# Optimization experiments

Hardware: AMD Instinct MI355X
Metric: run time of the kernel (lower is better)

## Reference

```python
import jax, jax.numpy as jnp
import numpy as np

B, T, D = 64, 512, 512
H, DH = 8, 64  # head_num, att_embedding_size; H*DH == D
NEG = jnp.float32(-2.0**32 + 1)


def _pos_encoding(t, d):
    # Position_Embedding (mode='sum'): [cos, sin] concat over d/2 frequencies
    inv_freq = 1.0 / jnp.power(10000.0, 2.0 * jnp.arange(d // 2, dtype=jnp.float32) / d)
    pij = jnp.arange(t, dtype=jnp.float32)[:, None] * inv_freq[None, :]  # (T, d/2)
    return jnp.concatenate([jnp.cos(pij), jnp.sin(pij)], axis=-1)  # (T, d)


def setup_inputs() -> dict:
    key = jax.random.key(0)
    ks = jax.random.split(key, 9)
    queries = jax.random.normal(ks[0], (B, T, D), dtype=jnp.float32)
    keys = jax.random.normal(ks[1], (B, T, D), dtype=jnp.float32)
    query_lens = jax.random.randint(ks[2], (B, 1), 1, T + 1)
    key_lens = jax.random.randint(ks[3], (B, 1), 1, T + 1)
    W_Q = jax.random.truncated_normal(ks[4], -2., 2., (D, H * DH), dtype=jnp.float32) * 0.05
    W_K = jax.random.truncated_normal(ks[5], -2., 2., (D, H * DH), dtype=jnp.float32) * 0.05
    W_V = jax.random.truncated_normal(ks[6], -2., 2., (D, H * DH), dtype=jnp.float32) * 0.05
    fw1 = jax.random.normal(ks[7], (H * DH, 4 * H * DH), dtype=jnp.float32) * 0.02
    fw2 = jax.random.normal(ks[8], (4 * H * DH, H * DH), dtype=jnp.float32) * 0.02
    return {"queries": queries, "keys": keys, "query_lens": query_lens,
            "key_lens": key_lens, "W_Q": W_Q, "W_K": W_K, "W_V": W_V,
            "fw1": fw1, "fw2": fw2}


def reference(queries, keys, query_lens, key_lens, W_Q, W_K, W_V, fw1, fw2):
    # sequence masks (B, T) from lengths (B, 1)
    ar = jnp.arange(T)
    q_mask = (ar[None, :] < query_lens).astype(jnp.float32)  # (B, T)
    k_mask = ar[None, :] < key_lens                          # (B, T) bool

    pe = _pos_encoding(T, D)[None]  # (1, T, D)
    q_in = queries + pe
    k_in = keys + pe

    qp = jnp.einsum('btd,de->bte', q_in, W_Q).reshape(B, T, H, DH)
    kp = jnp.einsum('btd,de->bte', k_in, W_K)
    # DeepCTR quirk: values projected from the already-projected keys
    vp = jnp.einsum('btd,de->bte', kp, W_V).reshape(B, T, H, DH)
    kp = kp.reshape(B, T, H, DH)

    scores = jnp.einsum('bthd,bshd->bhts', qp, kp) / jnp.sqrt(jnp.float32(DH))
    scores = jnp.where(k_mask[:, None, None, :], scores, NEG)
    scores = scores - jnp.max(scores, axis=-1, keepdims=True)
    attn = jax.nn.softmax(scores, axis=-1)
    attn = attn * q_mask[:, None, :, None]

    out = jnp.einsum('bhts,bshd->bthd', attn, vp).reshape(B, T, H * DH)
    result = out + q_in  # residual uses PE-augmented queries

    ff = jnp.einsum('btd,df->btf', jax.nn.relu(jnp.einsum('btd,df->btf', result, fw1)), fw2)
    result = result + ff

    return jnp.mean(result, axis=1, keepdims=True)  # (B, 1, D)
```

## Files before the change

kernel.cpp:

```cpp
#include <hip/hip_runtime.h>

typedef unsigned short u16;
typedef __attribute__((ext_vector_type(8))) short short8;
typedef __attribute__((ext_vector_type(4))) float floatx4;

#define QSCALE 0.1803368801111204f

__device__ __forceinline__ u16 f2bf(float x) {
  union { float f; unsigned u; } un; un.f = x;
  unsigned r = un.u + 0x7fffu + ((un.u >> 16) & 1u);
  return (u16)(r >> 16);
}
__device__ __forceinline__ float bf2f(u16 h) {
  union { unsigned u; float f; } un; un.u = ((unsigned)h) << 16;
  return un.f;
}
__device__ __forceinline__ void gld16(const u16* g, u16* l) {
  __builtin_amdgcn_global_load_lds((__attribute__((address_space(1))) void*)g,
                                   (__attribute__((address_space(3))) void*)l, 16, 0, 0);
}

__global__ __launch_bounds__(256) void wtrans_all(const float* __restrict__ W_Q,
                                                  const float* __restrict__ W_K,
                                                  const float* __restrict__ fw1,
                                                  u16* __restrict__ WqT, u16* __restrict__ WkT,
                                                  u16* __restrict__ F1T) {
  __shared__ float tile[32][33];
  int L = blockIdx.x;
  const float* in;
  u16* out;
  int N, bx, by;
  if (L < 256) { in = W_Q; out = WqT; N = 512; bx = L & 15; by = L >> 4; }
  else if (L < 512) { L -= 256; in = W_K; out = WkT; N = 512; bx = L & 15; by = L >> 4; }
  else { L -= 512; in = fw1; out = F1T; N = 2048; bx = L & 63; by = L >> 6; }
  int tx = threadIdx.x, ty = threadIdx.y;
  int n0 = bx * 32, k0 = by * 32;
#pragma unroll
  for (int i = 0; i < 4; i++) {
    int kk = ty + i * 8;
    tile[kk][tx] = in[(size_t)(k0 + kk) * N + n0 + tx];
  }
  __syncthreads();
#pragma unroll
  for (int i = 0; i < 4; i++) {
    int nn = ty + i * 8;
    out[(size_t)(n0 + nn) * 512 + k0 + tx] = f2bf(tile[tx][nn]);
  }
}

__global__ __launch_bounds__(256) void wkv_kernel(const float* __restrict__ WK,
                                                  const float* __restrict__ WV,
                                                  u16* __restrict__ WkvT) {
  __shared__ float Kt[32][36];
  __shared__ float Vt[32][36];
  int nt = blockIdx.x & 15, dt = blockIdx.x >> 4;
  int n0 = nt * 32, d0 = dt * 32;
  int tid = threadIdx.x;
  int flat = tid * 4;
  int i4 = flat >> 5, j4 = flat & 31;
  int tn = tid & 15, td = tid >> 4;
  float acc00 = 0.f, acc01 = 0.f, acc10 = 0.f, acc11 = 0.f;
  for (int e0 = 0; e0 < 512; e0 += 32) {
    __syncthreads();
    *(float4*)&Kt[i4][j4] = *(const float4*)&WK[(size_t)(d0 + i4) * 512 + e0 + j4];
    *(float4*)&Vt[i4][j4] = *(const float4*)&WV[(size_t)(e0 + i4) * 512 + n0 + j4];
    __syncthreads();
#pragma unroll 8
    for (int e = 0; e < 32; e++) {
      float k0v = Kt[td * 2][e], k1v = Kt[td * 2 + 1][e];
      float v0 = Vt[e][tn * 2], v1 = Vt[e][tn * 2 + 1];
      acc00 += k0v * v0; acc01 += k0v * v1;
      acc10 += k1v * v0; acc11 += k1v * v1;
    }
  }
  size_t o = (size_t)(n0 + tn * 2) * 512 + d0 + td * 2;
  WkvT[o] = f2bf(acc00);
  WkvT[o + 1] = f2bf(acc10);
  WkvT[o + 512] = f2bf(acc01);
  WkvT[o + 513] = f2bf(acc11);
}

__global__ __launch_bounds__(256) void pe_table_kernel(float* __restrict__ pet) {
  int flat = (blockIdx.x * 256 + threadIdx.x) * 4;
  int d0 = flat & 511;
  int t = flat >> 9;
  float pe[4];
#pragma unroll
  for (int i = 0; i < 4; i++) {
    int d = d0 + i;
    int j = (d < 256) ? d : d - 256;
    float f = exp2f((float)j * -0.05190512648f);
    float arg = (float)t * f;
    pe[i] = (d < 256) ? cosf(arg) : sinf(arg);
  }
  *(float4*)(pet + flat) = *(const float4*)pe;
}

__global__ __launch_bounds__(256) void pe_add_kernel(const float* __restrict__ q,
                                                     const float* __restrict__ k,
                                                     const float* __restrict__ pet,
                                                     u16* __restrict__ qb, u16* __restrict__ kb) {
  size_t flat = ((size_t)blockIdx.x * 256 + threadIdx.x) * 4;
  const float4 qv = *(const float4*)(q + flat);
  const float4 kv = *(const float4*)(k + flat);
  const float4 pv = *(const float4*)(pet + (flat & 262143));
  u16 qo[4], ko[4];
  qo[0] = f2bf(qv.x + pv.x); qo[1] = f2bf(qv.y + pv.y);
  qo[2] = f2bf(qv.z + pv.z); qo[3] = f2bf(qv.w + pv.w);
  ko[0] = f2bf(kv.x + pv.x); ko[1] = f2bf(kv.y + pv.y);
  ko[2] = f2bf(kv.z + pv.z); ko[3] = f2bf(kv.w + pv.w);
  *(uint2*)(qb + flat) = *(const uint2*)qo;
  *(uint2*)(kb + flat) = *(const uint2*)ko;
}

__global__ __launch_bounds__(512, 2) void proj_256(const u16* __restrict__ q_in,
                                                   const u16* __restrict__ k_in,
                                                   const u16* __restrict__ WqT,
                                                   const u16* __restrict__ WkT,
                                                   const u16* __restrict__ WkvT,
                                                   u16* __restrict__ qp,
                                                   u16* __restrict__ kpb,
                                                   u16* __restrict__ vTp) {
  __shared__ u16 lds[65536];
  const int K = 512;
  const int tid = threadIdx.x;
  const int lane = tid & 63, w = tid >> 6;
  const int quad = lane >> 4, cl = lane & 15;
  const int wm = w >> 2, wn = w & 3;
  int L = blockIdx.x;
  const int seg = L >> 8;
  L &= 255;
  const u16* A = (seg == 0) ? q_in : k_in;
  const u16* Bt = (seg == 0) ? WqT : (seg == 1) ? WkT : WkvT;
  const int xcd = L & 7, s = L >> 3;
  const int nx = s & 1;
  const int rgrp = s >> 1;
  const int tm = (rgrp * 8 + xcd) * 256;
  const int tn = nx * 256;
  const int srow = lane >> 3;
  const int sg = (lane & 7) ^ srow;
  const int cb = w * 4;

  floatx4 acc[8][4] = {};

  {
    u16* Ab = lds;
    u16* Bb = lds + 16384;
#pragma unroll
    for (int i = 0; i < 4; i++) {
      int cc = cb + i, row = cc * 8 + srow;
      gld16(A + ((size_t)(tm + row) * K + sg * 8), &Ab[cc * 512]);
    }
#pragma unroll
    for (int i = 0; i < 4; i++) {
      int cc = cb + i, row = cc * 8 + srow;
      gld16(Bt + ((size_t)(tn + row) * K + sg * 8), &Bb[cc * 512]);
    }
  }

  const int nk = K >> 6;
#pragma unroll 1
  for (int kt = 0; kt < nk; kt++) {
    u16* Ab = lds + (kt & 1) * 32768;
    u16* Bb = Ab + 16384;
    u16* An = lds + ((kt & 1) ^ 1) * 32768;
    u16* Bn = An + 16384;
    const bool pf = (kt + 1 < nk);
    const int k0n = (kt + 1) << 6;
    if (pf) {
#pragma unroll
      for (int i = 0; i < 4; i++) {
        int cc = cb + i, row = cc * 8 + srow;
        gld16(A + ((size_t)(tm + row) * K + k0n + sg * 8), &An[cc * 512]);
      }
#pragma unroll
      for (int i = 0; i < 4; i++) {
        int cc = cb + i, row = cc * 8 + srow;
        gld16(Bt + ((size_t)(tn + row) * K + k0n + sg * 8), &Bn[cc * 512]);
      }
      asm volatile("s_waitcnt vmcnt(8)" ::: "memory");
    } else {
      asm volatile("s_waitcnt vmcnt(0)" ::: "memory");
    }
    __builtin_amdgcn_s_barrier();
    __builtin_amdgcn_sched_barrier(0);
    short8 a0[4][2], b0[2][2], b1[2][2], a1[4][2];
#pragma unroll
    for (int f = 0; f < 4; f++)
#pragma unroll
      for (int kh = 0; kh < 2; kh++)
        a0[f][kh] = *(const short8*)&Ab[(wm * 128 + f * 16 + cl) * 64 + ((((kh << 2) + quad)) ^ (cl & 7)) * 8];
#pragma unroll
    for (int n = 0; n < 2; n++)
#pragma unroll
      for (int kh = 0; kh < 2; kh++)
        b0[n][kh] = *(const short8*)&Bb[(wn * 64 + n * 16 + cl) * 64 + ((((kh << 2) + quad)) ^ (cl & 7)) * 8];
#pragma unroll
    for (int f = 0; f < 4; f++)
#pragma unroll
      for (int n = 0; n < 2; n++)
#pragma unroll
        for (int kh = 0; kh < 2; kh++)
          acc[f][n] = __builtin_amdgcn_mfma_f32_16x16x32_bf16(a0[f][kh], b0[n][kh], acc[f][n], 0, 0, 0);
#pragma unroll
    for (int n = 0; n < 2; n++)
#pragma unroll
      for (int kh = 0; kh < 2; kh++)
        b1[n][kh] = *(const short8*)&Bb[(wn * 64 + (n + 2) * 16 + cl) * 64 + ((((kh << 2) + quad)) ^ (cl & 7)) * 8];
#pragma unroll
    for (int f = 0; f < 4; f++)
#pragma unroll
      for (int n = 0; n < 2; n++)
#pragma unroll
        for (int kh = 0; kh < 2; kh++)
          acc[f][n + 2] = __builtin_amdgcn_mfma_f32_16x16x32_bf16(a0[f][kh], b1[n][kh], acc[f][n + 2], 0, 0, 0);
#pragma unroll
    for (int f = 0; f < 4; f++)
#pragma unroll
      for (int kh = 0; kh < 2; kh++)
        a1[f][kh] = *(const short8*)&Ab[(wm * 128 + (f + 4) * 16 + cl) * 64 + ((((kh << 2) + quad)) ^ (cl & 7)) * 8];
#pragma unroll
    for (int f = 0; f < 4; f++)
#pragma unroll
      for (int n = 0; n < 2; n++)
#pragma unroll
        for (int kh = 0; kh < 2; kh++)
          acc[f + 4][n + 2] = __builtin_amdgcn_mfma_f32_16x16x32_bf16(a1[f][kh], b1[n][kh], acc[f + 4][n + 2], 0, 0, 0);
#pragma unroll
    for (int f = 0; f < 4; f++)
#pragma unroll
      for (int n = 0; n < 2; n++)
#pragma unroll
        for (int kh = 0; kh < 2; kh++)
          acc[f + 4][n] = __builtin_amdgcn_mfma_f32_16x16x32_bf16(a1[f][kh], b0[n][kh], acc[f + 4][n], 0, 0, 0);
    __builtin_amdgcn_s_barrier();
  }

  if (seg < 2) {
    u16* C = (seg == 0) ? qp : kpb;
#pragma unroll
    for (int f = 0; f < 8; f++)
#pragma unroll
      for (int n = 0; n < 4; n++)
#pragma unroll
        for (int r = 0; r < 4; r++) {
          int row = tm + wm * 128 + f * 16 + quad * 4 + r;
          int col = tn + wn * 64 + n * 16 + cl;
          C[(size_t)row * 512 + col] = f2bf(acc[f][n][r]);
        }
  } else {
    const int b = tm >> 9, sbase = tm & 511;
#pragma unroll 1
    for (int p = 0; p < 2; p++) {
      __syncthreads();
      if ((wn >> 1) == p) {
        int cbase = (wn & 1) * 64;
#pragma unroll
        for (int f = 0; f < 8; f++)
#pragma unroll
          for (int n = 0; n < 4; n++)
#pragma unroll
            for (int r = 0; r < 4; r++) {
              int tc = cbase + n * 16 + cl;
              int row = wm * 128 + f * 16 + quad * 4 + r;
              lds[tc * 264 + row] = f2bf(acc[f][n][r]);
            }
      }
      __syncthreads();
      int col = tid >> 2;
      int e = tn + p * 128 + col;
      int h = e >> 6, d = e & 63;
      u16* dst = vTp + ((size_t)((b * 8 + h) * 64 + d) * 512 + sbase);
#pragma unroll
      for (int j = 0; j < 8; j++) {
        int chunk = (tid & 3) + j * 4;
        *(short8*)(dst + chunk * 8) = *(const short8*)&lds[col * 264 + chunk * 8];
      }
    }
  }
}

__global__ __launch_bounds__(512, 2) void ffn1_256(const u16* __restrict__ A,
                                                   const u16* __restrict__ Bt,
                                                   float* __restrict__ outp) {
  __shared__ u16 lds[65536];
  const int K = 512;
  const int tid = threadIdx.x;
  const int lane = tid & 63, w = tid >> 6;
  const int quad = lane >> 4, cl = lane & 15;
  const int wm = w >> 2, wn = w & 3;
  int L = blockIdx.x;
  const int xcd = L & 7, s = L >> 3;
  const int nx = s & 7;
  const int rgrp = s >> 3;
  const int tm = (rgrp * 8 + xcd) * 256;
  const int tn = nx * 256;
  const int srow = lane >> 3;
  const int sg = (lane & 7) ^ srow;
  const int cb = w * 4;

  floatx4 acc[8][4] = {};

  {
    u16* Ab = lds;
    u16* Bb = lds + 16384;
#pragma unroll
    for (int i = 0; i < 4; i++) {
      int cc = cb + i, row = cc * 8 + srow;
      gld16(A + ((size_t)(tm + row) * K + sg * 8), &Ab[cc * 512]);
    }
#pragma unroll
    for (int i = 0; i < 4; i++) {
      int cc = cb + i, row = cc * 8 + srow;
      gld16(Bt + ((size_t)(tn + row) * K + sg * 8), &Bb[cc * 512]);
    }
  }

  const int nk = K >> 6;
#pragma unroll 1
  for (int kt = 0; kt < nk; kt++) {
    u16* Ab = lds + (kt & 1) * 32768;
    u16* Bb = Ab + 16384;
    u16* An = lds + ((kt & 1) ^ 1) * 32768;
    u16* Bn = An + 16384;
    const bool pf = (kt + 1 < nk);
    const int k0n = (kt + 1) << 6;
    if (pf) {
#pragma unroll
      for (int i = 0; i < 4; i++) {
        int cc = cb + i, row = cc * 8 + srow;
        gld16(A + ((size_t)(tm + row) * K + k0n + sg * 8), &An[cc * 512]);
      }
#pragma unroll
      for (int i = 0; i < 4; i++) {
        int cc = cb + i, row = cc * 8 + srow;
        gld16(Bt + ((size_t)(tn + row) * K + k0n + sg * 8), &Bn[cc * 512]);
      }
      asm volatile("s_waitcnt vmcnt(8)" ::: "memory");
    } else {
      asm volatile("s_waitcnt vmcnt(0)" ::: "memory");
    }
    __builtin_amdgcn_s_barrier();
    __builtin_amdgcn_sched_barrier(0);
    short8 a0[4][2], b0[2][2], b1[2][2], a1[4][2];
#pragma unroll
    for (int f = 0; f < 4; f++)
#pragma unroll
      for (int kh = 0; kh < 2; kh++)
        a0[f][kh] = *(const short8*)&Ab[(wm * 128 + f * 16 + cl) * 64 + ((((kh << 2) + quad)) ^ (cl & 7)) * 8];
#pragma unroll
    for (int n = 0; n < 2; n++)
#pragma unroll
      for (int kh = 0; kh < 2; kh++)
        b0[n][kh] = *(const short8*)&Bb[(wn * 64 + n * 16 + cl) * 64 + ((((kh << 2) + quad)) ^ (cl & 7)) * 8];
#pragma unroll
    for (int f = 0; f < 4; f++)
#pragma unroll
      for (int n = 0; n < 2; n++)
#pragma unroll
        for (int kh = 0; kh < 2; kh++)
          acc[f][n] = __builtin_amdgcn_mfma_f32_16x16x32_bf16(a0[f][kh], b0[n][kh], acc[f][n], 0, 0, 0);
#pragma unroll
    for (int n = 0; n < 2; n++)
#pragma unroll
      for (int kh = 0; kh < 2; kh++)
        b1[n][kh] = *(const short8*)&Bb[(wn * 64 + (n + 2) * 16 + cl) * 64 + ((((kh << 2) + quad)) ^ (cl & 7)) * 8];
#pragma unroll
    for (int f = 0; f < 4; f++)
#pragma unroll
      for (int n = 0; n < 2; n++)
#pragma unroll
        for (int kh = 0; kh < 2; kh++)
          acc[f][n + 2] = __builtin_amdgcn_mfma_f32_16x16x32_bf16(a0[f][kh], b1[n][kh], acc[f][n + 2], 0, 0, 0);
#pragma unroll
    for (int f = 0; f < 4; f++)
#pragma unroll
      for (int kh = 0; kh < 2; kh++)
        a1[f][kh] = *(const short8*)&Ab[(wm * 128 + (f + 4) * 16 + cl) * 64 + ((((kh << 2) + quad)) ^ (cl & 7)) * 8];
#pragma unroll
    for (int f = 0; f < 4; f++)
#pragma unroll
      for (int n = 0; n < 2; n++)
#pragma unroll
        for (int kh = 0; kh < 2; kh++)
          acc[f + 4][n + 2] = __builtin_amdgcn_mfma_f32_16x16x32_bf16(a1[f][kh], b1[n][kh], acc[f + 4][n + 2], 0, 0, 0);
#pragma unroll
    for (int f = 0; f < 4; f++)
#pragma unroll
      for (int n = 0; n < 2; n++)
#pragma unroll
        for (int kh = 0; kh < 2; kh++)
          acc[f + 4][n] = __builtin_amdgcn_mfma_f32_16x16x32_bf16(a1[f][kh], b0[n][kh], acc[f + 4][n], 0, 0, 0);
    __builtin_amdgcn_s_barrier();
  }

  float cs[4] = {0.f, 0.f, 0.f, 0.f};
#pragma unroll
  for (int f = 0; f < 8; f++)
#pragma unroll
    for (int n = 0; n < 4; n++)
#pragma unroll
      for (int r = 0; r < 4; r++) cs[n] += fmaxf(acc[f][n][r], 0.0f);
#pragma unroll
  for (int n = 0; n < 4; n++) {
    cs[n] += __shfl_xor(cs[n], 16);
    cs[n] += __shfl_xor(cs[n], 32);
  }
  if (quad == 0) {
    int b = tm >> 9;
#pragma unroll
    for (int n = 0; n < 4; n++)
      atomicAdd(outp + (size_t)b * 2048 + tn + wn * 64 + n * 16 + cl, cs[n]);
  }
}

__global__ __launch_bounds__(256) void ffn2_mean_kernel(const float* __restrict__ sums,
                                                        const float* __restrict__ fw2,
                                                        float* __restrict__ outp) {
  __shared__ float s[128];
  int fs = blockIdx.x & 15, b = blockIdx.x >> 4;
  int tid = threadIdx.x;
  if (tid < 128) s[tid] = sums[(size_t)b * 2048 + fs * 128 + tid];
  __syncthreads();
  const float* w = fw2 + (size_t)(fs * 128) * 512;
  float a0 = 0.f, a1 = 0.f;
#pragma unroll 4
  for (int f = 0; f < 128; f++) {
    float sv = s[f];
    a0 += sv * w[(size_t)f * 512 + tid];
    a1 += sv * w[(size_t)f * 512 + 256 + tid];
  }
  atomicAdd(outp + b * 512 + tid, a0 * (1.0f / 512.0f));
  atomicAdd(outp + b * 512 + 256 + tid, a1 * (1.0f / 512.0f));
}

__global__ __launch_bounds__(256) void attn_kernel(const u16* __restrict__ qp, const u16* __restrict__ kp,
                                                   const u16* __restrict__ vT, const u16* __restrict__ qin,
                                                   u16* __restrict__ resout, const int* __restrict__ qlen,
                                                   const int* __restrict__ klen, float* __restrict__ outp) {
  __shared__ u16 KPu[8704];
  __shared__ u16 Vlds[64 * 128];
  __shared__ float Csum[4][64];
  int L = blockIdx.x;
  int xcd = L & 7;
  int idx = L >> 3;
  int qt = idx & 7;
  int g = xcd + (idx >> 3) * 8;
  int h = g & 7, b = g >> 3;
  int tid = threadIdx.x, lane = tid & 63, w = tid >> 6;
  int quad = lane >> 4, cl = lane & 15;
  int kl = klen[b], ql = qlen[b];
  int q0 = qt * 64 + w * 16;

  if (qt * 64 >= ql) {
    int c = tid & 63, r0 = (tid >> 6) * 16;
    float sv = 0.f;
#pragma unroll
    for (int i = 0; i < 16; i++) {
      size_t idx2 = ((size_t)(b * 512 + qt * 64 + r0 + i) * 512) + h * 64 + c;
      u16 val = qin[idx2];
      resout[idx2] = val;
      sv += bf2f(val);
    }
    Csum[w][c] = sv;
    __syncthreads();
    if (tid < 64) {
      float t = Csum[0][tid] + Csum[1][tid] + Csum[2][tid] + Csum[3][tid];
      atomicAdd(outp + b * 512 + h * 64 + tid, t * (1.0f / 512.0f));
    }
    return;
  }
  bool wactive = q0 < ql;

  short8 qfrag[2];
#pragma unroll
  for (int ks = 0; ks < 2; ks++)
    qfrag[ks] = *(const short8*)(qp + ((size_t)(b * 512 + q0 + cl) * 512 + h * 64 + ks * 32 + quad * 8));
  const short8 ones8 = {(short)0x3F80, (short)0x3F80, (short)0x3F80, (short)0x3F80,
                        (short)0x3F80, (short)0x3F80, (short)0x3F80, (short)0x3F80};
  float m_r[4];
  floatx4 o[4] = {};
  floatx4 lacc = {};
#pragma unroll
  for (int r = 0; r < 4; r++) m_r[r] = -3.0e38f;

  int nkt = (kl + 127) >> 7;
  for (int kt = 0; kt < nkt; kt++) {
    __syncthreads();
#pragma unroll
    for (int i = 0; i < 4; i++) {
      int c = w * 4 + i;
      int row = c * 8 + (lane >> 3);
      int gc = (lane & 7) ^ (row & 7);
      gld16(kp + ((size_t)(b * 512 + kt * 128 + row) * 512 + h * 64 + gc * 8), &KPu[c * 512]);
    }
#pragma unroll
    for (int i = 0; i < 4; i++) {
      int c = w * 4 + i;
      int row = c * 4 + (lane >> 4);
      int gc = (lane & 15) ^ (row & 7);
      gld16(vT + ((size_t)((b * 8 + h) * 64 + row) * 512 + kt * 128 + gc * 8), &Vlds[c * 512]);
    }
    asm volatile("s_waitcnt vmcnt(4)" ::: "memory");
    __builtin_amdgcn_s_barrier();
    __builtin_amdgcn_sched_barrier(0);
    floatx4 sacc[8] = {};
    float mnew[4], alpha[4];
    if (wactive) {
      __builtin_amdgcn_s_setprio(1);
#pragma unroll
      for (int f = 0; f < 8; f++) {
        int krow = f * 16 + cl;
#pragma unroll
        for (int ks = 0; ks < 2; ks++) {
          int kc = ks * 4 + quad;
          short8 kf = *(const short8*)&KPu[krow * 64 + ((kc ^ (cl & 7)) * 8)];
          sacc[f] = __builtin_amdgcn_mfma_f32_16x16x32_bf16(qfrag[ks], kf, sacc[f], 0, 0, 0);
        }
      }
      __builtin_amdgcn_s_setprio(0);
#pragma unroll
      for (int r = 0; r < 4; r++) mnew[r] = m_r[r];
#pragma unroll
      for (int f = 0; f < 8; f++) {
        int key = kt * 128 + f * 16 + cl;
        bool ok = key < kl;
#pragma unroll
        for (int r = 0; r < 4; r++) {
          float v = ok ? sacc[f][r] * QSCALE : -4294967296.0f;
          sacc[f][r] = v;
          mnew[r] = fmaxf(mnew[r], v);
        }
      }
#pragma unroll
      for (int mk = 1; mk <= 8; mk <<= 1)
#pragma unroll
        for (int r = 0; r < 4; r++) mnew[r] = fmaxf(mnew[r], __shfl_xor(mnew[r], mk));
#pragma unroll
      for (int r = 0; r < 4; r++) {
        alpha[r] = exp2f(m_r[r] - mnew[r]);
        m_r[r] = mnew[r];
      }
    }
    __syncthreads();
    if (wactive) {
      u16* P = &KPu[w * 2176];
#pragma unroll
      for (int f = 0; f < 8; f++)
#pragma unroll
        for (int r = 0; r < 4; r++) {
          float p = exp2f(sacc[f][r] - mnew[r]);
          P[(quad * 4 + r) * 136 + f * 16 + cl] = f2bf(p);
        }
#pragma unroll
      for (int r = 0; r < 4; r++) lacc[r] *= alpha[r];
#pragma unroll
      for (int fd = 0; fd < 4; fd++)
#pragma unroll
        for (int r = 0; r < 4; r++) o[fd][r] *= alpha[r];
      __builtin_amdgcn_s_setprio(1);
#pragma unroll
      for (int k2 = 0; k2 < 4; k2++) {
        short8 pf = *(const short8*)&P[cl * 136 + k2 * 32 + quad * 8];
        lacc = __builtin_amdgcn_mfma_f32_16x16x32_bf16(pf, ones8, lacc, 0, 0, 0);
#pragma unroll
        for (int fd = 0; fd < 4; fd++) {
          int vrow = fd * 16 + cl;
          int sc = k2 * 4 + quad;
          short8 vf = *(const short8*)&Vlds[vrow * 128 + ((sc ^ (cl & 7)) * 8)];
          o[fd] = __builtin_amdgcn_mfma_f32_16x16x32_bf16(pf, vf, o[fd], 0, 0, 0);
        }
      }
      __builtin_amdgcn_s_setprio(0);
    }
  }
  float colsum[4] = {0.f, 0.f, 0.f, 0.f};
#pragma unroll
  for (int fd = 0; fd < 4; fd++)
#pragma unroll
    for (int r = 0; r < 4; r++) {
      int q = q0 + quad * 4 + r;
      float v = o[fd][r] / lacc[r];
      if (q >= ql) v = 0.f;
      size_t idx2 = (size_t)(b * 512 + q) * 512 + h * 64 + fd * 16 + cl;
      v += bf2f(qin[idx2]);
      resout[idx2] = f2bf(v);
      colsum[fd] += v;
    }
#pragma unroll
  for (int fd = 0; fd < 4; fd++) {
    colsum[fd] += __shfl_xor(colsum[fd], 16);
    colsum[fd] += __shfl_xor(colsum[fd], 32);
  }
  if (quad == 0) {
#pragma unroll
    for (int fd = 0; fd < 4; fd++) Csum[w][fd * 16 + cl] = colsum[fd];
  }
  __syncthreads();
  if (tid < 64) {
    float t = Csum[0][tid] + Csum[1][tid] + Csum[2][tid] + Csum[3][tid];
    atomicAdd(outp + b * 512 + h * 64 + tid, t * (1.0f / 512.0f));
  }
}

extern "C" void kernel_launch(void* const* d_in, const int* in_sizes, int n_in,
                              void* d_out, int out_size, void* d_ws, size_t ws_size,
                              hipStream_t stream) {
  const float* queries = (const float*)d_in[0];
  const float* keys = (const float*)d_in[1];
  const int* qlen = (const int*)d_in[2];
  const int* klen = (const int*)d_in[3];
  const float* W_Q = (const float*)d_in[4];
  const float* W_K = (const float*)d_in[5];
  const float* W_V = (const float*)d_in[6];
  const float* fw1 = (const float*)d_in[7];
  const float* fw2 = (const float*)d_in[8];
  float* outp = (float*)d_out;
  char* ws = (char*)d_ws;

  constexpr size_t SZ_W = 512 * 512 * 2;
  constexpr size_t SZ_F = 2048 * 512 * 2;
  constexpr size_t SZ_S = 64 * 2048 * 4;
  constexpr size_t SZ_T = (size_t)64 * 512 * 512 * 2;
  size_t o_WqT = 0;
  size_t o_WkT = o_WqT + SZ_W;
  size_t o_Wkv = o_WkT + SZ_W;
  size_t o_F1T = o_Wkv + SZ_W;
  size_t o_SUM = o_F1T + SZ_F;
  size_t o_ABCD = o_SUM + SZ_S;
  size_t o_E = o_ABCD + 4 * SZ_T;
  size_t NEED = o_E + SZ_T;
  if (ws_size < NEED) return;

  u16* WqT = (u16*)(ws + o_WqT);
  u16* WkT = (u16*)(ws + o_WkT);
  u16* WkvT = (u16*)(ws + o_Wkv);
  u16* F1T = (u16*)(ws + o_F1T);
  float* sums = (float*)(ws + o_SUM);
  u16* q_in = (u16*)(ws + o_ABCD);
  u16* k_in = (u16*)(ws + o_ABCD + SZ_T);
  u16* qp = (u16*)(ws + o_ABCD + 2 * SZ_T);
  u16* kpb = (u16*)(ws + o_ABCD + 3 * SZ_T);
  u16* vT = (u16*)(ws + o_E);
  float* pet = (float*)(ws + o_E);
  u16* resb = k_in;

  hipMemsetAsync(d_out, 0, (size_t)out_size * sizeof(float), stream);
  hipMemsetAsync(sums, 0, SZ_S, stream);

  wtrans_all<<<1536, dim3(32, 8), 0, stream>>>(W_Q, W_K, fw1, WqT, WkT, F1T);
  wkv_kernel<<<256, 256, 0, stream>>>(W_K, W_V, WkvT);
  pe_table_kernel<<<256, 256, 0, stream>>>(pet);
  pe_add_kernel<<<16384, 256, 0, stream>>>(queries, keys, pet, q_in, k_in);

  proj_256<<<768, 512, 0, stream>>>(q_in, k_in, WqT, WkT, WkvT, qp, kpb, vT);

  attn_kernel<<<4096, 256, 0, stream>>>(qp, kpb, vT, q_in, resb, qlen, klen, outp);

  ffn1_256<<<1024, 512, 0, stream>>>(resb, F1T, sums);
  ffn2_mean_kernel<<<1024, 256, 0, stream>>>(sums, fw2, outp);
}
```

Before: 391.0 us.

## Interleave half-tile global prefetch with MFMA phases in 256x256 GEMM k-loop

Factors the shared 256x256 bf16 GEMM main loop into a helper used by both the projection and FFN kernels. The loop now issues next-tile global-to-LDS loads in four quarter chunks spread across the four MFMA sub-phases, with barriers and fine-grained vmcnt waits between phases, and raises wave priority around the MFMA bursts. The aim is to hide global load latency and smooth memory traffic rather than issue all prefetches at loop start. It adds more barriers per iteration and relies on precise waitcnt accounting, which risks sync overhead or races if the counts are wrong.

```diff
diff --git a/kernel.cpp b/kernel.cpp
--- a/kernel.cpp
+++ b/kernel.cpp
@@ -113,6 +113,141 @@
   *(uint2*)(kb + flat) = *(const uint2*)ko;
 }
 
+template <int HT>
+__device__ __forceinline__ void stage_half(const u16* M, int tbase, int k0, u16* buf,
+                                           int w, int lane) {
+  const int srow = lane >> 3;
+  const int sg = (lane & 7) ^ srow;
+#pragma unroll
+  for (int i = 0; i < 2; i++) {
+    int j = w * 2 + i;
+    int row0;
+    if constexpr (HT == 0) row0 = j * 8 + ((j >= 8) ? 64 : 0);
+    else if constexpr (HT == 3) row0 = j * 8 + ((j >= 8) ? 64 : 0) + 64;
+    else if constexpr (HT == 1) row0 = (j >> 2) * 64 + (j & 3) * 8;
+    else row0 = (j >> 2) * 64 + 32 + (j & 3) * 8;
+    gld16(M + ((size_t)(tbase + row0 + srow) * 512 + k0 + sg * 8), &buf[row0 * 64]);
+  }
+}
+
+__device__ __forceinline__ void kloop256(const u16* __restrict__ A, const u16* __restrict__ Bt,
+                                         int tm, int tn, u16* lds, int tid,
+                                         floatx4 (&acc)[8][4]) {
+  const int lane = tid & 63, w = tid >> 6;
+  const int quad = lane >> 4, cl = lane & 15;
+  const int wm = w >> 2, wn = w & 3;
+  const int nk = 8;
+
+  stage_half<0>(A, tm, 0, lds, w, lane);
+  stage_half<1>(Bt, tn, 0, lds + 16384, w, lane);
+  stage_half<2>(Bt, tn, 0, lds + 16384, w, lane);
+  stage_half<3>(A, tm, 0, lds, w, lane);
+  asm volatile("s_waitcnt vmcnt(4)" ::: "memory");
+  __builtin_amdgcn_s_barrier();
+
+#pragma unroll 1
+  for (int kt = 0; kt < nk; kt++) {
+    u16* Ab = lds + (kt & 1) * 32768;
+    u16* Bb = Ab + 16384;
+    u16* An = lds + ((kt & 1) ^ 1) * 32768;
+    u16* Bn = An + 16384;
+    const bool pf = (kt + 1 < nk);
+    const int k0n = (kt + 1) << 6;
+    short8 a0[4][2], a1[4][2], b0[2][2], b1[2][2];
+
+#pragma unroll
+    for (int f = 0; f < 4; f++)
+#pragma unroll
+      for (int kh = 0; kh < 2; kh++)
+        a0[f][kh] = *(const short8*)&Ab[(wm * 128 + f * 16 + cl) * 64 + ((((kh << 2) + quad)) ^ (cl & 7)) * 8];
+#pragma unroll
+    for (int n = 0; n < 2; n++)
+#pragma unroll
+      for (int kh = 0; kh < 2; kh++)
+        b0[n][kh] = *(const short8*)&Bb[(wn * 64 + n * 16 + cl) * 64 + ((((kh << 2) + quad)) ^ (cl & 7)) * 8];
+    if (pf) {
+      stage_half<0>(A, tm, k0n, An, w, lane);
+      asm volatile("s_waitcnt vmcnt(4)" ::: "memory");
+    } else {
+      asm volatile("s_waitcnt vmcnt(2)" ::: "memory");
+    }
+    __builtin_amdgcn_s_barrier();
+    asm volatile("s_waitcnt lgkmcnt(0)" ::: "memory");
+    __builtin_amdgcn_sched_barrier(0);
+    __builtin_amdgcn_s_setprio(1);
+#pragma unroll
+    for (int f = 0; f < 4; f++)
+#pragma unroll
+      for (int n = 0; n < 2; n++)
+#pragma unroll
+        for (int kh = 0; kh < 2; kh++)
+          acc[f][n] = __builtin_amdgcn_mfma_f32_16x16x32_bf16(a0[f][kh], b0[n][kh], acc[f][n], 0, 0, 0);
+    __builtin_amdgcn_s_setprio(0);
+    __builtin_amdgcn_s_barrier();
+
+#pragma unroll
+    for (int n = 0; n < 2; n++)
+#pragma unroll
+      for (int kh = 0; kh < 2; kh++)
+        b1[n][kh] = *(const short8*)&Bb[(wn * 64 + (n + 2) * 16 + cl) * 64 + ((((kh << 2) + quad)) ^ (cl & 7)) * 8];
+    if (pf) {
+      stage_half<1>(Bt, tn, k0n, Bn, w, lane);
+      asm volatile("s_waitcnt vmcnt(4)" ::: "memory");
+    } else {
+      asm volatile("s_waitcnt vmcnt(0)" ::: "memory");
+    }
+    __builtin_amdgcn_s_barrier();
+    asm volatile("s_waitcnt lgkmcnt(0)" ::: "memory");
+    __builtin_amdgcn_sched_barrier(0);
+    __builtin_amdgcn_s_setprio(1);
+#pragma unroll
+    for (int f = 0; f < 4; f++)
+#pragma unroll
+      for (int n = 0; n < 2; n++)
+#pragma unroll
+        for (int kh = 0; kh < 2; kh++)
+          acc[f][n + 2] = __builtin_amdgcn_mfma_f32_16x16x32_bf16(a0[f][kh], b1[n][kh], acc[f][n + 2], 0, 0, 0);
+    __builtin_amdgcn_s_setprio(0);
+    __builtin_amdgcn_s_barrier();
+
+#pragma unroll
+    for (int f = 0; f < 4; f++)
+#pragma unroll
+      for (int kh = 0; kh < 2; kh++)
+        a1[f][kh] = *(const short8*)&Ab[(wm * 128 + (f + 4) * 16 + cl) * 64 + ((((kh << 2) + quad)) ^ (cl & 7)) * 8];
+    if (pf) stage_half<2>(Bt, tn, k0n, Bn, w, lane);
+    __builtin_amdgcn_s_barrier();
+    asm volatile("s_waitcnt lgkmcnt(0)" ::: "memory");
+    __builtin_amdgcn_sched_barrier(0);
+    __builtin_amdgcn_s_setprio(1);
+#pragma unroll
+    for (int f = 0; f < 4; f++)
+#pragma unroll
+      for (int n = 0; n < 2; n++)
+#pragma unroll
+        for (int kh = 0; kh < 2; kh++)
+          acc[f + 4][n + 2] = __builtin_amdgcn_mfma_f32_16x16x32_bf16(a1[f][kh], b1[n][kh], acc[f + 4][n + 2], 0, 0, 0);
+    __builtin_amdgcn_s_setprio(0);
+    __builtin_amdgcn_s_barrier();
+
+    if (pf) {
+      stage_half<3>(A, tm, k0n, An, w, lane);
+      asm volatile("s_waitcnt vmcnt(4)" ::: "memory");
+    }
+    __builtin_amdgcn_s_barrier();
+    __builtin_amdgcn_s_setprio(1);
+#pragma unroll
+    for (int f = 0; f < 4; f++)
+#pragma unroll
+      for (int n = 0; n < 2; n++)
+#pragma unroll
+        for (int kh = 0; kh < 2; kh++)
+          acc[f + 4][n] = __builtin_amdgcn_mfma_f32_16x16x32_bf16(a1[f][kh], b0[n][kh], acc[f + 4][n], 0, 0, 0);
+    __builtin_amdgcn_s_setprio(0);
+    __builtin_amdgcn_s_barrier();
+  }
+}
+
 __global__ __launch_bounds__(512, 2) void proj_256(const u16* __restrict__ q_in,
                                                    const u16* __restrict__ k_in,
                                                    const u16* __restrict__ WqT,
@@ -122,7 +257,6 @@
                                                    u16* __restrict__ kpb,
                                                    u16* __restrict__ vTp) {
   __shared__ u16 lds[65536];
-  const int K = 512;
   const int tid = threadIdx.x;
   const int lane = tid & 63, w = tid >> 6;
   const int quad = lane >> 4, cl = lane & 15;
@@ -137,104 +271,9 @@
   const int rgrp = s >> 1;
   const int tm = (rgrp * 8 + xcd) * 256;
   const int tn = nx * 256;
-  const int srow = lane >> 3;
-  const int sg = (lane & 7) ^ srow;
-  const int cb = w * 4;
 
   floatx4 acc[8][4] = {};
-
-  {
-    u16* Ab = lds;
-    u16* Bb = lds + 16384;
-#pragma unroll
-    for (int i = 0; i < 4; i++) {
-      int cc = cb + i, row = cc * 8 + srow;
-      gld16(A + ((size_t)(tm + row) * K + sg * 8), &Ab[cc * 512]);
-    }
-#pragma unroll
-    for (int i = 0; i < 4; i++) {
-      int cc = cb + i, row = cc * 8 + srow;
-      gld16(Bt + ((size_t)(tn + row) * K + sg * 8), &Bb[cc * 512]);
-    }
-  }
-
-  const int nk = K >> 6;
-#pragma unroll 1
-  for (int kt = 0; kt < nk; kt++) {
-    u16* Ab = lds + (kt & 1) * 32768;
-    u16* Bb = Ab + 16384;
-    u16* An = lds + ((kt & 1) ^ 1) * 32768;
-    u16* Bn = An + 16384;
-    const bool pf = (kt + 1 < nk);
-    const int k0n = (kt + 1) << 6;
-    if (pf) {
-#pragma unroll
-      for (int i = 0; i < 4; i++) {
-        int cc = cb + i, row = cc * 8 + srow;
-        gld16(A + ((size_t)(tm + row) * K + k0n + sg * 8), &An[cc * 512]);
-      }
-#pragma unroll
-      for (int i = 0; i < 4; i++) {
-        int cc = cb + i, row = cc * 8 + srow;
-        gld16(Bt + ((size_t)(tn + row) * K + k0n + sg * 8), &Bn[cc * 512]);
-      }
-      asm volatile("s_waitcnt vmcnt(8)" ::: "memory");
-    } else {
-      asm volatile("s_waitcnt vmcnt(0)" ::: "memory");
-    }
-    __builtin_amdgcn_s_barrier();
-    __builtin_amdgcn_sched_barrier(0);
-    short8 a0[4][2], b0[2][2], b1[2][2], a1[4][2];
-#pragma unroll
-    for (int f = 0; f < 4; f++)
-#pragma unroll
-      for (int kh = 0; kh < 2; kh++)
-        a0[f][kh] = *(const short8*)&Ab[(wm * 128 + f * 16 + cl) * 64 + ((((kh << 2) + quad)) ^ (cl & 7)) * 8];
-#pragma unroll
-    for (int n = 0; n < 2; n++)
-#pragma unroll
-      for (int kh = 0; kh < 2; kh++)
-        b0[n][kh] = *(const short8*)&Bb[(wn * 64 + n * 16 + cl) * 64 + ((((kh << 2) + quad)) ^ (cl & 7)) * 8];
-#pragma unroll
-    for (int f = 0; f < 4; f++)
-#pragma unroll
-      for (int n = 0; n < 2; n++)
-#pragma unroll
-        for (int kh = 0; kh < 2; kh++)
-          acc[f][n] = __builtin_amdgcn_mfma_f32_16x16x32_bf16(a0[f][kh], b0[n][kh], acc[f][n], 0, 0, 0);
-#pragma unroll
-    for (int n = 0; n < 2; n++)
-#pragma unroll
-      for (int kh = 0; kh < 2; kh++)
-        b1[n][kh] = *(const short8*)&Bb[(wn * 64 + (n + 2) * 16 + cl) * 64 + ((((kh << 2) + quad)) ^ (cl & 7)) * 8];
-#pragma unroll
-    for (int f = 0; f < 4; f++)
-#pragma unroll
-      for (int n = 0; n < 2; n++)
-#pragma unroll
-        for (int kh = 0; kh < 2; kh++)
-          acc[f][n + 2] = __builtin_amdgcn_mfma_f32_16x16x32_bf16(a0[f][kh], b1[n][kh], acc[f][n + 2], 0, 0, 0);
-#pragma unroll
-    for (int f = 0; f < 4; f++)
-#pragma unroll
-      for (int kh = 0; kh < 2; kh++)
-        a1[f][kh] = *(const short8*)&Ab[(wm * 128 + (f + 4) * 16 + cl) * 64 + ((((kh << 2) + quad)) ^ (cl & 7)) * 8];
-#pragma unroll
-    for (int f = 0; f < 4; f++)
-#pragma unroll
-      for (int n = 0; n < 2; n++)
-#pragma unroll
-        for (int kh = 0; kh < 2; kh++)
-          acc[f + 4][n + 2] = __builtin_amdgcn_mfma_f32_16x16x32_bf16(a1[f][kh], b1[n][kh], acc[f + 4][n + 2], 0, 0, 0);
-#pragma unroll
-    for (int f = 0; f < 4; f++)
-#pragma unroll
-      for (int n = 0; n < 2; n++)
-#pragma unroll
-        for (int kh = 0; kh < 2; kh++)
-          acc[f + 4][n] = __builtin_amdgcn_mfma_f32_16x16x32_bf16(a1[f][kh], b0[n][kh], acc[f + 4][n], 0, 0, 0);
-    __builtin_amdgcn_s_barrier();
-  }
+  kloop256(A, Bt, tm, tn, lds, tid, acc);
 
   if (seg < 2) {
     u16* C = (seg == 0) ? qp : kpb;
@@ -284,115 +323,19 @@
                                                    const u16* __restrict__ Bt,
                                                    float* __restrict__ outp) {
   __shared__ u16 lds[65536];
-  const int K = 512;
   const int tid = threadIdx.x;
   const int lane = tid & 63, w = tid >> 6;
   const int quad = lane >> 4, cl = lane & 15;
-  const int wm = w >> 2, wn = w & 3;
+  const int wn = w & 3;
   int L = blockIdx.x;
   const int xcd = L & 7, s = L >> 3;
   const int nx = s & 7;
   const int rgrp = s >> 3;
   const int tm = (rgrp * 8 + xcd) * 256;
   const int tn = nx * 256;
-  const int srow = lane >> 3;
-  const int sg = (lane & 7) ^ srow;
-  const int cb = w * 4;
 
   floatx4 acc[8][4] = {};
-
-  {
-    u16* Ab = lds;
-    u16* Bb = lds + 16384;
-#pragma unroll
-    for (int i = 0; i < 4; i++) {
-      int cc = cb + i, row = cc * 8 + srow;
-      gld16(A + ((size_t)(tm + row) * K + sg * 8), &Ab[cc * 512]);
-    }
-#pragma unroll
-    for (int i = 0; i < 4; i++) {
-      int cc = cb + i, row = cc * 8 + srow;
-      gld16(Bt + ((size_t)(tn + row) * K + sg * 8), &Bb[cc * 512]);
-    }
-  }
-
-  const int nk = K >> 6;
-#pragma unroll 1
-  for (int kt = 0; kt < nk; kt++) {
-    u16* Ab = lds + (kt & 1) * 32768;
-    u16* Bb = Ab + 16384;
-    u16* An = lds + ((kt & 1) ^ 1) * 32768;
-    u16* Bn = An + 16384;
-    const bool pf = (kt + 1 < nk);
-    const int k0n = (kt + 1) << 6;
-    if (pf) {
-#pragma unroll
-      for (int i = 0; i < 4; i++) {
-        int cc = cb + i, row = cc * 8 + srow;
-        gld16(A + ((size_t)(tm + row) * K + k0n + sg * 8), &An[cc * 512]);
-      }
-#pragma unroll
-      for (int i = 0; i < 4; i++) {
-        int cc = cb + i, row = cc * 8 + srow;
-        gld16(Bt + ((size_t)(tn + row) * K + k0n + sg * 8), &Bn[cc * 512]);
-      }
-      asm volatile("s_waitcnt vmcnt(8)" ::: "memory");
-    } else {
-      asm volatile("s_waitcnt vmcnt(0)" ::: "memory");
-    }
-    __builtin_amdgcn_s_barrier();
-    __builtin_amdgcn_sched_barrier(0);
-    short8 a0[4][2], b0[2][2], b1[2][2], a1[4][2];
-#pragma unroll
-    for (int f = 0; f < 4; f++)
-#pragma unroll
-      for (int kh = 0; kh < 2; kh++)
-        a0[f][kh] = *(const short8*)&Ab[(wm * 128 + f * 16 + cl) * 64 + ((((kh << 2) + quad)) ^ (cl & 7)) * 8];
-#pragma unroll
-    for (int n = 0; n < 2; n++)
-#pragma unroll
-      for (int kh = 0; kh < 2; kh++)
-        b0[n][kh] = *(const short8*)&Bb[(wn * 64 + n * 16 + cl) * 64 + ((((kh << 2) + quad)) ^ (cl & 7)) * 8];
-#pragma unroll
-    for (int f = 0; f < 4; f++)
-#pragma unroll
-      for (int n = 0; n < 2; n++)
-#pragma unroll
-        for (int kh = 0; kh < 2; kh++)
-          acc[f][n] = __builtin_amdgcn_mfma_f32_16x16x32_bf16(a0[f][kh], b0[n][kh], acc[f][n], 0, 0, 0);
-#pragma unroll
-    for (int n = 0; n < 2; n++)
-#pragma unroll
-      for (int kh = 0; kh < 2; kh++)
-        b1[n][kh] = *(const short8*)&Bb[(wn * 64 + (n + 2) * 16 + cl) * 64 + ((((kh << 2) + quad)) ^ (cl & 7)) * 8];
-#pragma unroll
-    for (int f = 0; f < 4; f++)
-#pragma unroll
-      for (int n = 0; n < 2; n++)
-#pragma unroll
-        for (int kh = 0; kh < 2; kh++)
-          acc[f][n + 2] = __builtin_amdgcn_mfma_f32_16x16x32_bf16(a0[f][kh], b1[n][kh], acc[f][n + 2], 0, 0, 0);
-#pragma unroll
-    for (int f = 0; f < 4; f++)
-#pragma unroll
-      for (int kh = 0; kh < 2; kh++)
-        a1[f][kh] = *(const short8*)&Ab[(wm * 128 + (f + 4) * 16 + cl) * 64 + ((((kh << 2) + quad)) ^ (cl & 7)) * 8];
-#pragma unroll
-    for (int f = 0; f < 4; f++)
-#pragma unroll
-      for (int n = 0; n < 2; n++)
-#pragma unroll
-        for (int kh = 0; kh < 2; kh++)
-          acc[f + 4][n + 2] = __builtin_amdgcn_mfma_f32_16x16x32_bf16(a1[f][kh], b1[n][kh], acc[f + 4][n + 2], 0, 0, 0);
-#pragma unroll
-    for (int f = 0; f < 4; f++)
-#pragma unroll
-      for (int n = 0; n < 2; n++)
-#pragma unroll
-        for (int kh = 0; kh < 2; kh++)
-          acc[f + 4][n] = __builtin_amdgcn_mfma_f32_16x16x32_bf16(a1[f][kh], b0[n][kh], acc[f + 4][n], 0, 0, 0);
-    __builtin_amdgcn_s_barrier();
-  }
+  kloop256(A, Bt, tm, tn, lds, tid, acc);
 
   float cs[4] = {0.f, 0.f, 0.f, 0.f};
 #pragma unroll
```

Result: no change. 397.0 us (+1.5%).
